# Kernel optimization log

Measured on AMD Instinct MI355X. Metric: run time of the kernel, lower is better.

Reference implementation:

```python
import jax, jax.numpy as jnp
import numpy as np

STEP = 16      # step_size
WIN = 8        # causal window width from attn_mask
NUM_HEADS = 4
LN_EPS = 1e-5


def conv1d(x, w, b, pad, dil):
    # x: [B, Cin, T], w: [Cout, Cin, K] (torch layout)
    y = jax.lax.conv_general_dilated(
        x, w, window_strides=(1,), padding=[(pad, pad)],
        rhs_dilation=(dil,), dimension_numbers=('NCH', 'OIH', 'NCH'))
    return y + b[None, :, None]


def temporal_block(x, w1, b1, w2, b2, wd, bd, dil, pad):
    # Canonical TCN block: conv->chomp->relu (dropout=eval noop) x2 + residual
    T = x.shape[-1]
    out = jax.nn.relu(conv1d(x, w1, b1, pad, dil)[..., :T])
    out = jax.nn.relu(conv1d(out, w2, b2, pad, dil)[..., :T])
    res = x if wd is None else conv1d(x, wd, bd, 0, 1)
    return jax.nn.relu(out + res)


def layer_norm(x, g, b):
    m = x.mean(-1, keepdims=True)
    v = x.var(-1, keepdims=True)
    return (x - m) / jnp.sqrt(v + LN_EPS) * g + b


def setup_inputs() -> dict:
    key = jax.random.key(0)
    NOISE, HID, B, T = 128, 256, 32, 4096
    ks = iter(jax.random.split(key, 48))
    rn = lambda shape, s=0.05: jax.random.normal(next(ks), shape, jnp.float32) * s
    inp = {'z': jax.random.normal(next(ks), (B, NOISE, T), jnp.float32)}
    # TCN block 0: kernel 1, noise_dim -> hidden_dim, with 1x1 downsample
    inp['tb0_w1'] = rn((HID, NOISE, 1)); inp['tb0_b1'] = jnp.zeros(HID)
    inp['tb0_w2'] = rn((HID, HID, 1));   inp['tb0_b2'] = jnp.zeros(HID)
    inp['tb0_wd'] = rn((HID, NOISE, 1)); inp['tb0_bd'] = jnp.zeros(HID)
    # TCN blocks 1..3: kernel 2, dilations 1,2,4, same channels (identity residual)
    for i in (1, 2, 3):
        inp[f'tb{i}_w1'] = rn((HID, HID, 2)); inp[f'tb{i}_b1'] = jnp.zeros(HID)
        inp[f'tb{i}_w2'] = rn((HID, HID, 2)); inp[f'tb{i}_b2'] = jnp.zeros(HID)
    # MultiheadAttention params (torch layout)
    inp['attn_in_w'] = rn((3 * HID, HID)); inp['attn_in_b'] = jnp.zeros(3 * HID)
    inp['attn_out_w'] = rn((HID, HID));    inp['attn_out_b'] = jnp.zeros(HID)
    inp['ln1_g'] = jnp.ones(HID); inp['ln1_b'] = jnp.zeros(HID)
    inp['ln2_g'] = jnp.ones(HID); inp['ln2_b'] = jnp.zeros(HID)
    inp['ffn_w1'] = rn((2 * HID, HID)); inp['ffn_b1'] = jnp.zeros(2 * HID)
    inp['ffn_w2'] = rn((HID, 2 * HID)); inp['ffn_b2'] = jnp.zeros(HID)
    inp['last_w'] = rn((1, HID)); inp['last_b'] = jnp.zeros(1)
    return inp


def reference(z, tb0_w1, tb0_b1, tb0_w2, tb0_b2, tb0_wd, tb0_bd,
              tb1_w1, tb1_b1, tb1_w2, tb1_b2,
              tb2_w1, tb2_b1, tb2_w2, tb2_b2,
              tb3_w1, tb3_b1, tb3_w2, tb3_b2,
              attn_in_w, attn_in_b, attn_out_w, attn_out_b,
              ln1_g, ln1_b, ln2_g, ln2_b,
              ffn_w1, ffn_b1, ffn_w2, ffn_b2,
              last_w, last_b):
    # --- TCN stack ---
    z = temporal_block(z, tb0_w1, tb0_b1, tb0_w2, tb0_b2, tb0_wd, tb0_bd, 1, 0)
    z = temporal_block(z, tb1_w1, tb1_b1, tb1_w2, tb1_b2, None, None, 1, 1)
    z = temporal_block(z, tb2_w1, tb2_b1, tb2_w2, tb2_b2, None, None, 2, 2)
    z = temporal_block(z, tb3_w1, tb3_b1, tb3_w2, tb3_b2, None, None, 4, 4)
    B, C, T = z.shape
    S = T // STEP
    # [B,C,S,STEP] -> [B,STEP,S,C] -> [B*STEP, S, C]
    x = z.reshape(B, C, S, STEP).transpose(0, 3, 2, 1).reshape(B * STEP, S, C)
    # --- causal sliding-window MHA ---
    qkv = x @ attn_in_w.T + attn_in_b
    q, k, v = jnp.split(qkv, 3, axis=-1)
    H, Dh = NUM_HEADS, C // NUM_HEADS
    heads = lambda t: t.reshape(B * STEP, S, H, Dh).transpose(0, 2, 1, 3)
    q, k, v = heads(q), heads(k), heads(v)
    scale = 1.0 / float(np.sqrt(Dh))
    scores = jnp.einsum('bhqd,bhkd->bhqk', q, k) * scale
    i = jnp.arange(S)[:, None]; j = jnp.arange(S)[None, :]
    allowed = (i - j >= 0) & (i - j < WIN)   # masked where i-j<0 or i-j>=8
    scores = jnp.where(allowed, scores, -jnp.inf)
    attn = jax.nn.softmax(scores, axis=-1)
    o = jnp.einsum('bhqk,bhkd->bhqd', attn, v)
    o = o.transpose(0, 2, 1, 3).reshape(B * STEP, S, C)
    o = o @ attn_out_w.T + attn_out_b
    # --- residual + LN + FFN + LN (dropout = eval noop) ---
    x = layer_norm(x + o, ln1_g, ln1_b)
    f = jax.nn.gelu(x @ ffn_w1.T + ffn_b1, approximate=False) @ ffn_w2.T + ffn_b2
    x = layer_norm(x + f, ln2_g, ln2_b)
    # un-fold back to [B, C, T]
    z = x.reshape(B, STEP, S, C).transpose(0, 3, 2, 1).reshape(B, C, T)
    out = z.transpose(0, 2, 1) @ last_w.T + last_b  # [B, T, 1]
    return out.transpose(0, 2, 1)                    # [B, 1, T]
```

## Files before the change

kernel.cpp:

```cpp
#include <hip/hip_runtime.h>
#include <cmath>

#define BB 32
#define TT 4096

typedef unsigned short u16;
typedef __attribute__((ext_vector_type(8))) __bf16 bf16x8;
typedef __attribute__((ext_vector_type(4))) float f32x4;
typedef __attribute__((ext_vector_type(8))) unsigned short u16x8;
typedef __attribute__((ext_vector_type(4))) unsigned short u16x4;
typedef __attribute__((ext_vector_type(2))) unsigned short u16x2;
typedef __attribute__((ext_vector_type(4))) unsigned int u32x4;

typedef __attribute__((address_space(3))) unsigned int lds_uint;
typedef __attribute__((address_space(1))) unsigned int g_uint;

__device__ __forceinline__ void gl_lds16(const void* g, void* l) {
    __builtin_amdgcn_global_load_lds((const g_uint*)g, (lds_uint*)l, 16, 0, 0);
}

__device__ __forceinline__ u16 f2b(float x) {
    unsigned u = __builtin_bit_cast(unsigned, x);
    return (u16)((u + 0x7fffu + ((u >> 16) & 1u)) >> 16);
}
__device__ __forceinline__ float b2f(u16 h) {
    unsigned u = ((unsigned)h) << 16;
    return __builtin_bit_cast(float, u);
}
__device__ __forceinline__ unsigned pkbf(float a, float b) {
    unsigned ua = __builtin_bit_cast(unsigned, a) + 0x8000u;
    unsigned ub = __builtin_bit_cast(unsigned, b) + 0x8000u;
    return __builtin_amdgcn_perm(ub, ua, 0x07060302);
}

enum : int {
  W_TB0_1 = 0,
  W_TB0_2 = 32768,
  W_TB0_D = 98304,
  W_TB1_1_T0 = 131072, W_TB1_1_T1 = 196608,
  W_TB1_2_T0 = 262144, W_TB1_2_T1 = 327680,
  W_TB2_1_T0 = 393216, W_TB2_1_T1 = 458752,
  W_TB2_2_T0 = 524288, W_TB2_2_T1 = 589824,
  W_TB3_1_T0 = 655360, W_TB3_1_T1 = 720896,
  W_TB3_2_T0 = 786432, W_TB3_2_T1 = 851968,
  W_ATTN_IN  = 917504,
  W_ATTN_OUT = 1114112,
  W_FFN1     = 1179648,
  W_FFN2     = 1310720,
};

__global__ __launch_bounds__(256)
void prep_weights(const float* s0, const float* s1, const float* s2,
                  const float* s3, const float* s4, const float* s5,
                  const float* s6, const float* s7, const float* s8,
                  const float* s9, const float* s10, const float* s11,
                  const float* s12, u16* wb)
{
    int seg = blockIdx.y;
    int i = blockIdx.x * 256 + threadIdx.x;
    switch (seg) {
    case 0:  if (i < 32768)  wb[W_TB0_1 + i] = f2b(s0[i]); break;
    case 1:  if (i < 65536)  wb[W_TB0_2 + i] = f2b(s1[i]); break;
    case 2:  if (i < 32768)  wb[W_TB0_D + i] = f2b(s2[i]); break;
    case 3:  if (i < 65536) { wb[W_TB1_1_T0 + i] = f2b(s3[2*i]); wb[W_TB1_1_T1 + i] = f2b(s3[2*i+1]); } break;
    case 4:  if (i < 65536) { wb[W_TB1_2_T0 + i] = f2b(s4[2*i]); wb[W_TB1_2_T1 + i] = f2b(s4[2*i+1]); } break;
    case 5:  if (i < 65536) { wb[W_TB2_1_T0 + i] = f2b(s5[2*i]); wb[W_TB2_1_T1 + i] = f2b(s5[2*i+1]); } break;
    case 6:  if (i < 65536) { wb[W_TB2_2_T0 + i] = f2b(s6[2*i]); wb[W_TB2_2_T1 + i] = f2b(s6[2*i+1]); } break;
    case 7:  if (i < 65536) { wb[W_TB3_1_T0 + i] = f2b(s7[2*i]); wb[W_TB3_1_T1 + i] = f2b(s7[2*i+1]); } break;
    case 8:  if (i < 65536) { wb[W_TB3_2_T0 + i] = f2b(s8[2*i]); wb[W_TB3_2_T1 + i] = f2b(s8[2*i+1]); } break;
    case 9:  if (i < 196608) wb[W_ATTN_IN + i]  = f2b(s9[i]);  break;
    case 10: if (i < 65536)  wb[W_ATTN_OUT + i] = f2b(s10[i]); break;
    case 11: if (i < 131072) wb[W_FFN1 + i]     = f2b(s11[i]); break;
    case 12: if (i < 131072) wb[W_FFN2 + i]     = f2b(s12[i]); break;
    }
}

__global__ __launch_bounds__(256)
void transpose_z(const float* __restrict__ z, u16* __restrict__ Z)
{
    __shared__ u16 tile[64][33];
    const int t0 = blockIdx.x << 6;
    const int c0 = blockIdx.y << 5;
    const int b  = blockIdx.z;
    const int tid = threadIdx.x;
    #pragma unroll
    for (int r = 0; r < 8; r++) {
        int lin = r * 256 + tid;
        int cc = lin >> 6, tt = lin & 63;
        tile[tt][cc] = f2b(z[((size_t)b * 128 + c0 + cc) * TT + t0 + tt]);
    }
    __syncthreads();
    #pragma unroll
    for (int r = 0; r < 8; r++) {
        int lin = r * 256 + tid;
        int tt = lin >> 5, cc = lin & 31;
        Z[((size_t)b * TT + t0 + tt) * 128 + c0 + cc] = tile[tt][cc];
    }
}

__device__ __forceinline__ const bf16x8* lds_frag(const u16* base, int row, int lc) {
    return (const bf16x8*)((const char*)base + row * 128 + (((lc ^ row) & 7) << 4) + ((lc & ~7) << 4));
}

template<int ACT, int RMODE, int EPI>
__global__ __launch_bounds__(256)
void gemm64(const u16* __restrict__ X, const u16* __restrict__ W, int K, int M,
            const float* __restrict__ bias,
            const u16* __restrict__ res, u16* __restrict__ Y,
            const float* __restrict__ g, const float* __restrict__ be,
            const float* __restrict__ lw, const float* __restrict__ lb,
            float* __restrict__ out)
{
    __shared__ __align__(16) char smem[40960];
    u16* Xs = (u16*)smem;
    u16* Ws = (u16*)(smem + 8192);
    float (*CT)[260] = (float(*)[260])smem;

    const int tid = threadIdx.x;
    const int b  = blockIdx.z;
    const int t0 = blockIdx.x << 6;
    const int n0 = blockIdx.y << 8;
    const int lane = tid & 63;
    const int wv = tid >> 6;
    const int wn = wv << 6;
    const int l15 = lane & 15;
    const int quad = lane >> 4;

    const char* xsrc[2]; char* xdst[2];
    #pragma unroll
    for (int u = 0; u < 2; u++) {
        const int c = tid + (u << 8);
        const int r = c >> 3, q = (c & 7) ^ (r & 7);
        xdst[u] = (char*)Xs + c * 16;
        xsrc[u] = (const char*)(X + ((size_t)b * TT + t0 + r) * K + q * 8);
    }
    const char* wsrc[8]; char* wdst[8];
    #pragma unroll
    for (int u = 0; u < 8; u++) {
        const int c = tid + (u << 8);
        const int r = c >> 3, q = (c & 7) ^ (r & 7);
        wdst[u] = (char*)Ws + c * 16;
        wsrc[u] = (const char*)(W + (size_t)(n0 + r) * K + q * 8);
    }

    f32x4 acc[4][4];
    #pragma unroll
    for (int j = 0; j < 4; j++) {
        const f32x4 bj = *(const f32x4*)&bias[n0 + wn + j * 16 + quad * 4];
        #pragma unroll
        for (int i = 0; i < 4; i++) acc[i][j] = bj;
    }

    for (int k0 = 0; k0 < K; k0 += 64) {
        #pragma unroll
        for (int u = 0; u < 2; u++) gl_lds16(xsrc[u] + 2 * k0, xdst[u]);
        #pragma unroll
        for (int u = 0; u < 8; u++) gl_lds16(wsrc[u] + 2 * k0, wdst[u]);
        __syncthreads();
        #pragma unroll
        for (int ks = 0; ks < 2; ks++) {
            const int lc = ks * 4 + quad;
            bf16x8 af[4], bw[4];
            #pragma unroll
            for (int i = 0; i < 4; i++)
                af[i] = *lds_frag(Xs, i * 16 + l15, lc);
            #pragma unroll
            for (int j = 0; j < 4; j++)
                bw[j] = *lds_frag(Ws, wn + j * 16 + l15, lc);
            #pragma unroll
            for (int i = 0; i < 4; i++)
                #pragma unroll
                for (int j = 0; j < 4; j++)
                    acc[i][j] = __builtin_amdgcn_mfma_f32_16x16x32_bf16(bw[j], af[i], acc[i][j], 0, 0, 0);
        }
        __syncthreads();
    }

    #pragma unroll
    for (int h = 0; h < 2; h++) {
        #pragma unroll
        for (int i2 = 0; i2 < 2; i2++) {
            const int tt = i2 * 16 + l15;
            #pragma unroll
            for (int j = 0; j < 4; j++) {
                const int c = wn + j * 16 + quad * 4;
                const int pc = (c + 8 * tt) & 255;
                *(f32x4*)&CT[tt][pc] = acc[h * 2 + i2][j];
            }
        }
        __syncthreads();
        #pragma unroll
        for (int r4 = 0; r4 < 4; r4++) {
            const int lin = (r4 << 8) + tid;
            const int tt = lin >> 5;
            const int ck = lin & 31;
            const int pcc = ((ck + tt) & 31) << 3;
            const int token = t0 + h * 32 + tt;
            const int gc = n0 + ck * 8;
            f32x4 v0 = *(const f32x4*)&CT[tt][pcc];
            f32x4 v1 = *(const f32x4*)&CT[tt][pcc + 4];
            if (RMODE == 1 || EPI >= 1) {
                const u16x8 rv = *(const u16x8*)&res[((size_t)b * TT + token) * 256 + ck * 8];
                #pragma unroll
                for (int e = 0; e < 4; e++) { v0[e] += b2f(rv[e]); v1[e] += b2f(rv[e + 4]); }
            }
            if (EPI == 0) {
                if (ACT == 1) {
                    #pragma unroll
                    for (int e = 0; e < 4; e++) { v0[e] = fmaxf(v0[e], 0.f); v1[e] = fmaxf(v1[e], 0.f); }
                }
                if (ACT == 2) {
                    #pragma unroll
                    for (int e = 0; e < 4; e++) {
                        v0[e] = 0.5f * v0[e] * (1.f + erff(v0[e] * 0.70710678118f));
                        v1[e] = 0.5f * v1[e] * (1.f + erff(v1[e] * 0.70710678118f));
                    }
                }
                u32x4 po;
                po[0] = pkbf(v0[0], v0[1]); po[1] = pkbf(v0[2], v0[3]);
                po[2] = pkbf(v1[0], v1[1]); po[3] = pkbf(v1[2], v1[3]);
                *(u32x4*)&Y[((size_t)b * TT + token) * M + gc] = po;
            } else {
                float s = 0.f, sq = 0.f;
                #pragma unroll
                for (int e = 0; e < 4; e++) {
                    s += v0[e] + v1[e];
                    sq += v0[e] * v0[e] + v1[e] * v1[e];
                }
                #pragma unroll
                for (int off = 16; off >= 1; off >>= 1) {
                    s += __shfl_xor(s, off, 64);
                    sq += __shfl_xor(sq, off, 64);
                }
                const float mean = s * (1.f / 256.f);
                const float var = sq * (1.f / 256.f) - mean * mean;
                const float rstd = rsqrtf(var + 1e-5f);
                const f32x4 g0 = *(const f32x4*)&g[gc];
                const f32x4 g1 = *(const f32x4*)&g[gc + 4];
                const f32x4 be0 = *(const f32x4*)&be[gc];
                const f32x4 be1 = *(const f32x4*)&be[gc + 4];
                f32x4 x0, x1;
                #pragma unroll
                for (int e = 0; e < 4; e++) {
                    x0[e] = (v0[e] - mean) * rstd * g0[e] + be0[e];
                    x1[e] = (v1[e] - mean) * rstd * g1[e] + be1[e];
                }
                if (EPI == 1) {
                    u32x4 po;
                    po[0] = pkbf(x0[0], x0[1]); po[1] = pkbf(x0[2], x0[3]);
                    po[2] = pkbf(x1[0], x1[1]); po[3] = pkbf(x1[2], x1[3]);
                    *(u32x4*)&Y[((size_t)b * TT + token) * 256 + gc] = po;
                } else {
                    const f32x4 w0 = *(const f32x4*)&lw[gc];
                    const f32x4 w1 = *(const f32x4*)&lw[gc + 4];
                    float a = 0.f;
                    #pragma unroll
                    for (int e = 0; e < 4; e++) a += x0[e] * w0[e] + x1[e] * w1[e];
                    #pragma unroll
                    for (int off = 16; off >= 1; off >>= 1) a += __shfl_xor(a, off, 64);
                    if ((lane & 31) == 0) out[(size_t)b * TT + token] = a + lb[0];
                }
            }
        }
        __syncthreads();
    }
}

template<int RMODE>
__global__ __launch_bounds__(256)
void gemm_dual(const u16* __restrict__ X, const u16* __restrict__ W1, int K,
               const u16* __restrict__ W2, int sh,
               const float* __restrict__ bias1,
               const u16* __restrict__ res, u16* __restrict__ Y,
               const u16* __restrict__ zp)
{
    constexpr int XR = 132;
    constexpr int STB = (XR + 256) * 128;
    constexpr int SMB = STB > 33792 ? STB : 33792;
    __shared__ __align__(16) char smem[SMB];
    u16* Xs = (u16*)smem;
    u16* Ws = (u16*)(smem + XR * 128);
    float (*CT)[132] = (float(*)[132])smem;

    const int tid = threadIdx.x;
    const int b  = blockIdx.z;
    const int t0 = blockIdx.x << 7;
    const int n0 = blockIdx.y << 7;
    const int lane = tid & 63;
    const int wv = tid >> 6;
    const int wt = (wv >> 1) << 6;
    const int wn = (wv & 1) << 6;
    const int l15 = lane & 15;
    const int quad = lane >> 4;
    const int shl = sh;

    const char* xsrc[4]; char* xdst[4];
    #pragma unroll
    for (int u = 0; u < 4; u++) {
        const int c = tid + (u << 8);
        const int r = c >> 3, p = c & 7, q = p ^ (r & 7);
        const int st = t0 + r - shl;
        xdst[u] = (char*)Xs + c * 16;
        xsrc[u] = (const char*)((st >= 0 ? (X + ((size_t)b * TT + st) * K) : zp) + q * 8);
    }
    const char* wsrc[8]; char* wdst[8];
    #pragma unroll
    for (int u = 0; u < 8; u++) {
        const int c = tid + (u << 8);
        const int r = c >> 3, p = c & 7, q = p ^ (r & 7);
        wdst[u] = (char*)Ws + c * 16;
        const u16* wb_ = (r >= 128) ? (W2 + (size_t)(n0 + r - 128) * K)
                                    : (W1 + (size_t)(n0 + r) * K);
        wsrc[u] = (const char*)(wb_ + q * 8);
    }
    const u16* hsrc = nullptr; u16* hdst = nullptr;
    if (tid < 8 * shl) {
        const int hr = 128 + (tid >> 3), hp = tid & 7, hq = hp ^ (hr & 7);
        hsrc = X + ((size_t)b * TT + t0 + hr - shl) * K + hq * 8;
        hdst = (u16*)((char*)Xs + (1024 + tid) * 16);
    }

    f32x4 acc[4][4];
    #pragma unroll
    for (int j = 0; j < 4; j++) {
        const f32x4 bj = *(const f32x4*)&bias1[n0 + wn + j * 16 + quad * 4];
        #pragma unroll
        for (int i = 0; i < 4; i++) acc[i][j] = bj;
    }

    for (int k0 = 0; k0 < K; k0 += 64) {
        #pragma unroll
        for (int u = 0; u < 4; u++) gl_lds16(xsrc[u] + 2 * k0, xdst[u]);
        #pragma unroll
        for (int u = 0; u < 8; u++) gl_lds16(wsrc[u] + 2 * k0, wdst[u]);
        if (hdst) *(u16x8*)hdst = *(const u16x8*)(hsrc + k0);
        __syncthreads();
        #pragma unroll
        for (int ks = 0; ks < 2; ks++) {
            bf16x8 af[4], bw[4];
            const int lc = ks * 4 + quad;
            #pragma unroll
            for (int i = 0; i < 4; i++)
                af[i] = *lds_frag(Xs, shl + wt + i * 16 + l15, lc);
            #pragma unroll
            for (int j = 0; j < 4; j++)
                bw[j] = *lds_frag(Ws, wn + j * 16 + l15, lc);
            #pragma unroll
            for (int i = 0; i < 4; i++)
                #pragma unroll
                for (int j = 0; j < 4; j++)
                    acc[i][j] = __builtin_amdgcn_mfma_f32_16x16x32_bf16(bw[j], af[i], acc[i][j], 0, 0, 0);
            #pragma unroll
            for (int i = 0; i < 4; i++)
                af[i] = *lds_frag(Xs, wt + i * 16 + l15, lc);
            #pragma unroll
            for (int j = 0; j < 4; j++)
                bw[j] = *lds_frag(Ws, 128 + wn + j * 16 + l15, lc);
            #pragma unroll
            for (int i = 0; i < 4; i++)
                #pragma unroll
                for (int j = 0; j < 4; j++)
                    acc[i][j] = __builtin_amdgcn_mfma_f32_16x16x32_bf16(bw[j], af[i], acc[i][j], 0, 0, 0);
        }
        __syncthreads();
    }

    #pragma unroll
    for (int h = 0; h < 2; h++) {
        if (wt == h * 64) {
            #pragma unroll
            for (int i = 0; i < 4; i++) {
                const int tt = i * 16 + l15;
                #pragma unroll
                for (int j = 0; j < 4; j++)
                    *(f32x4*)&CT[tt][wn + j * 16 + quad * 4] = acc[i][j];
            }
        }
        __syncthreads();
        #pragma unroll
        for (int r4 = 0; r4 < 4; r4++) {
            const int lin = (r4 << 8) + tid;
            const int tt = lin >> 4;
            const int ck = lin & 15;
            const int gr = t0 + h * 64 + tt;
            const int gc = n0 + ck * 8;
            const size_t oidx = ((size_t)b * TT + gr) * 256 + gc;
            f32x4 v0 = *(const f32x4*)&CT[tt][ck * 8];
            f32x4 v1 = *(const f32x4*)&CT[tt][ck * 8 + 4];
            if (RMODE == 2) {
                const u16x8 rv = *(const u16x8*)&res[oidx];
                #pragma unroll
                for (int e = 0; e < 4; e++) {
                    v0[e] = fmaxf(fmaxf(v0[e], 0.f) + b2f(rv[e]), 0.f);
                    v1[e] = fmaxf(fmaxf(v1[e], 0.f) + b2f(rv[e + 4]), 0.f);
                }
            } else {
                #pragma unroll
                for (int e = 0; e < 4; e++) { v0[e] = fmaxf(v0[e], 0.f); v1[e] = fmaxf(v1[e], 0.f); }
            }
            u32x4 po;
            po[0] = pkbf(v0[0], v0[1]); po[1] = pkbf(v0[2], v0[3]);
            po[2] = pkbf(v1[0], v1[1]); po[3] = pkbf(v1[2], v1[3]);
            *(u32x4*)&Y[oidx] = po;
        }
        if (h == 0) __syncthreads();
    }
}

__global__ __launch_bounds__(256)
void attn_win(const u16* __restrict__ QKV, u16* __restrict__ O)
{
    __shared__ u16 KV[256 * 68];
    const int p = blockIdx.x, h = blockIdx.y, b = blockIdx.z;
    const int tid = threadIdx.x;
    const int s = tid;

    float qv[64];
    {
        size_t qg = ((size_t)b * TT + s * 16 + p) * 768 + h * 64;
        #pragma unroll
        for (int c = 0; c < 8; c++) {
            u16x8 u = *(const u16x8*)&QKV[qg + c * 8];
            #pragma unroll
            for (int j = 0; j < 8; j++) qv[c * 8 + j] = b2f(u[j]);
        }
    }
    for (int u = tid; u < 2048; u += 256) {
        int r = u >> 3, q = u & 7;
        size_t g = ((size_t)b * TT + r * 16 + p) * 768 + 256 + h * 64 + q * 8;
        u16x8 v = *(const u16x8*)&QKV[g];
        u16x4 lo = {v[0], v[1], v[2], v[3]}, hi = {v[4], v[5], v[6], v[7]};
        *(u16x4*)&KV[r * 68 + q * 8] = lo;
        *(u16x4*)&KV[r * 68 + q * 8 + 4] = hi;
    }
    __syncthreads();
    float sc[8];
    float mx = -1e30f;
    #pragma unroll
    for (int kk = 0; kk < 8; kk++) {
        int row = s - 7 + kk;
        float a = -1e30f;
        if (row >= 0) {
            a = 0.f;
            const u16* kr = &KV[row * 68];
            #pragma unroll
            for (int d = 0; d < 32; d++) {
                u16x2 u = *(const u16x2*)&kr[d * 2];
                a += qv[d * 2] * b2f(u[0]) + qv[d * 2 + 1] * b2f(u[1]);
            }
            a *= 0.125f;
        }
        sc[kk] = a;
        mx = fmaxf(mx, a);
    }
    float se = 0.f;
    #pragma unroll
    for (int kk = 0; kk < 8; kk++) {
        float e = (sc[kk] > -1e29f) ? __expf(sc[kk] - mx) : 0.f;
        sc[kk] = e; se += e;
    }
    const float inv = 1.f / se;
    __syncthreads();
    for (int u = tid; u < 2048; u += 256) {
        int r = u >> 3, q = u & 7;
        size_t g = ((size_t)b * TT + r * 16 + p) * 768 + 512 + h * 64 + q * 8;
        u16x8 v = *(const u16x8*)&QKV[g];
        u16x4 lo = {v[0], v[1], v[2], v[3]}, hi = {v[4], v[5], v[6], v[7]};
        *(u16x4*)&KV[r * 68 + q * 8] = lo;
        *(u16x4*)&KV[r * 68 + q * 8 + 4] = hi;
    }
    __syncthreads();
    float ov[64];
    #pragma unroll
    for (int d = 0; d < 64; d++) ov[d] = 0.f;
    #pragma unroll
    for (int kk = 0; kk < 8; kk++) {
        int row = s - 7 + kk;
        if (row >= 0) {
            float w = sc[kk] * inv;
            const u16* vr = &KV[row * 68];
            #pragma unroll
            for (int d = 0; d < 32; d++) {
                u16x2 u = *(const u16x2*)&vr[d * 2];
                ov[d * 2]     += w * b2f(u[0]);
                ov[d * 2 + 1] += w * b2f(u[1]);
            }
        }
    }
    size_t og = ((size_t)b * TT + s * 16 + p) * 256 + h * 64;
    #pragma unroll
    for (int d4 = 0; d4 < 16; d4++) {
        u16x4 o = {f2b(ov[d4 * 4]), f2b(ov[d4 * 4 + 1]), f2b(ov[d4 * 4 + 2]), f2b(ov[d4 * 4 + 3])};
        *(u16x4*)&O[og + d4 * 4] = o;
    }
}

extern "C" void kernel_launch(void* const* d_in, const int* in_sizes, int n_in,
                              void* d_out, int out_size, void* d_ws, size_t ws_size,
                              hipStream_t stream)
{
    const float* z        = (const float*)d_in[0];
    const float* tb0_b1   = (const float*)d_in[2];
    const float* tb0_b2   = (const float*)d_in[4];
    const float* tb0_bd   = (const float*)d_in[6];
    const float* tb1_b1   = (const float*)d_in[8];
    const float* tb1_b2   = (const float*)d_in[10];
    const float* tb2_b1   = (const float*)d_in[12];
    const float* tb2_b2   = (const float*)d_in[14];
    const float* tb3_b1   = (const float*)d_in[16];
    const float* tb3_b2   = (const float*)d_in[18];
    const float* attn_in_b  = (const float*)d_in[20];
    const float* attn_out_b = (const float*)d_in[22];
    const float* ln1_g = (const float*)d_in[23];
    const float* ln1_b = (const float*)d_in[24];
    const float* ln2_g = (const float*)d_in[25];
    const float* ln2_b = (const float*)d_in[26];
    const float* ffn_b1 = (const float*)d_in[28];
    const float* ffn_b2 = (const float*)d_in[30];
    const float* last_w = (const float*)d_in[31];
    const float* last_b = (const float*)d_in[32];
    (void)in_sizes; (void)n_in; (void)out_size;

    const size_t MB = 1ull << 20;
    int Bc = 0;
    for (int c = 32; c >= 1; c >>= 1) {
        if (ws_size >= (4 + 12 * (size_t)c) * MB) { Bc = c; break; }
    }
    if (Bc == 0) return;

    char* ws = (char*)d_ws;
    u16* WBp = (u16*)ws;
    u16* zp  = (u16*)(ws + 3 * MB);
    u16* U1  = (u16*)(ws + 4 * MB);
    u16* U2  = (u16*)(ws + (4 + 2 * (size_t)Bc) * MB);
    u16* U3  = (u16*)(ws + (4 + 4 * (size_t)Bc) * MB);
    u16* Q   = (u16*)(ws + (4 + 6 * (size_t)Bc) * MB);
    u16* Z   = Q;
    u16* F   = Q;
    float* outp = (float*)d_out;

    dim3 b256(256);
    hipMemsetAsync((void*)zp, 0, 4096, stream);
    prep_weights<<<dim3(768, 13), b256, 0, stream>>>(
        (const float*)d_in[1], (const float*)d_in[3], (const float*)d_in[5],
        (const float*)d_in[7], (const float*)d_in[9], (const float*)d_in[11],
        (const float*)d_in[13], (const float*)d_in[15], (const float*)d_in[17],
        (const float*)d_in[19], (const float*)d_in[21],
        (const float*)d_in[27], (const float*)d_in[29], WBp);

    const int nchunk = 32 / Bc;
    for (int c = 0; c < nchunk; c++) {
        const float* zc = z + (size_t)c * Bc * 128 * TT;
        float* oc = outp + (size_t)c * Bc * TT;

        transpose_z<<<dim3(64, 4, Bc), b256, 0, stream>>>(zc, Z);

        gemm64<1, 0, 0><<<dim3(64, 1, Bc), b256, 0, stream>>>(Z, WBp + W_TB0_1, 128, 256,
            tb0_b1, nullptr, U1, nullptr, nullptr, nullptr, nullptr, nullptr);
        gemm64<1, 0, 0><<<dim3(64, 1, Bc), b256, 0, stream>>>(U1, WBp + W_TB0_2, 256, 256,
            tb0_b2, nullptr, U2, nullptr, nullptr, nullptr, nullptr, nullptr);
        gemm64<1, 1, 0><<<dim3(64, 1, Bc), b256, 0, stream>>>(Z, WBp + W_TB0_D, 128, 256,
            tb0_bd, U2, U3, nullptr, nullptr, nullptr, nullptr, nullptr);
        gemm_dual<0><<<dim3(32, 2, Bc), b256, 0, stream>>>(U3, WBp + W_TB1_1_T1, 256,
            WBp + W_TB1_1_T0, 1, tb1_b1, nullptr, U1, zp);
        gemm_dual<2><<<dim3(32, 2, Bc), b256, 0, stream>>>(U1, WBp + W_TB1_2_T1, 256,
            WBp + W_TB1_2_T0, 1, tb1_b2, U3, U2, zp);
        gemm_dual<0><<<dim3(32, 2, Bc), b256, 0, stream>>>(U2, WBp + W_TB2_1_T1, 256,
            WBp + W_TB2_1_T0, 2, tb2_b1, nullptr, U1, zp);
        gemm_dual<2><<<dim3(32, 2, Bc), b256, 0, stream>>>(U1, WBp + W_TB2_2_T1, 256,
            WBp + W_TB2_2_T0, 2, tb2_b2, U2, U3, zp);
        gemm_dual<0><<<dim3(32, 2, Bc), b256, 0, stream>>>(U3, WBp + W_TB3_1_T1, 256,
            WBp + W_TB3_1_T0, 4, tb3_b1, nullptr, U1, zp);
        gemm_dual<2><<<dim3(32, 2, Bc), b256, 0, stream>>>(U1, WBp + W_TB3_2_T1, 256,
            WBp + W_TB3_2_T0, 4, tb3_b2, U3, U2, zp);
        gemm64<0, 0, 0><<<dim3(64, 3, Bc), b256, 0, stream>>>(U2, WBp + W_ATTN_IN, 256, 768,
            attn_in_b, nullptr, Q, nullptr, nullptr, nullptr, nullptr, nullptr);
        attn_win<<<dim3(16, 4, Bc), b256, 0, stream>>>(Q, U3);
        gemm64<0, 0, 1><<<dim3(64, 1, Bc), b256, 0, stream>>>(U3, WBp + W_ATTN_OUT, 256, 256,
            attn_out_b, U2, U1, ln1_g, ln1_b, nullptr, nullptr, nullptr);
        gemm64<2, 0, 0><<<dim3(64, 2, Bc), b256, 0, stream>>>(U1, WBp + W_FFN1, 256, 512,
            ffn_b1, nullptr, F, nullptr, nullptr, nullptr, nullptr, nullptr);
        gemm64<0, 0, 2><<<dim3(64, 1, Bc), b256, 0, stream>>>(F, WBp + W_FFN2, 512, 256,
            ffn_b2, U1, nullptr, ln2_g, ln2_b, last_w, last_b, oc);
    }
}
```

Before: 912.0 us.

## Load GEMM fragments directly from global memory and merge dual-tap conv kernel

Replaces the LDS-staged async global-to-LDS tiling with direct per-lane global loads of MFMA fragments, fully unrolled over a compile-time K. It also folds the two-tap dilated conv kernel into the same templated GEMM, which now uses 64-token tiles and reads a shifted X row for the second tap. The aim is to drop LDS staging and barriers from the main loop. In exchange, global loads are uncoalesced across lanes and weights are re-read per wave with no shared reuse, so it leans heavily on cache.

```diff
diff --git a/kernel.cpp b/kernel.cpp
--- a/kernel.cpp
+++ b/kernel.cpp
@@ -11,13 +11,6 @@
 typedef __attribute__((ext_vector_type(4))) unsigned short u16x4;
 typedef __attribute__((ext_vector_type(2))) unsigned short u16x2;
 typedef __attribute__((ext_vector_type(4))) unsigned int u32x4;
-
-typedef __attribute__((address_space(3))) unsigned int lds_uint;
-typedef __attribute__((address_space(1))) unsigned int g_uint;
-
-__device__ __forceinline__ void gl_lds16(const void* g, void* l) {
-    __builtin_amdgcn_global_load_lds((const g_uint*)g, (lds_uint*)l, 16, 0, 0);
-}
 
 __device__ __forceinline__ u16 f2b(float x) {
     unsigned u = __builtin_bit_cast(unsigned, x);
@@ -98,23 +91,17 @@
     }
 }
 
-__device__ __forceinline__ const bf16x8* lds_frag(const u16* base, int row, int lc) {
-    return (const bf16x8*)((const char*)base + row * 128 + (((lc ^ row) & 7) << 4) + ((lc & ~7) << 4));
-}
-
-template<int ACT, int RMODE, int EPI>
+template<int ACT, int RMODE, int EPI, bool DUAL, int KT>
 __global__ __launch_bounds__(256)
-void gemm64(const u16* __restrict__ X, const u16* __restrict__ W, int K, int M,
-            const float* __restrict__ bias,
-            const u16* __restrict__ res, u16* __restrict__ Y,
-            const float* __restrict__ g, const float* __restrict__ be,
-            const float* __restrict__ lw, const float* __restrict__ lb,
-            float* __restrict__ out)
+void gemmd(const u16* __restrict__ X, const u16* __restrict__ W1, int M,
+           const u16* __restrict__ W2, int sh,
+           const float* __restrict__ bias,
+           const u16* __restrict__ res, u16* __restrict__ Y,
+           const float* __restrict__ g, const float* __restrict__ be,
+           const float* __restrict__ lw, const float* __restrict__ lb,
+           float* __restrict__ out, const u16* __restrict__ zp)
 {
-    __shared__ __align__(16) char smem[40960];
-    u16* Xs = (u16*)smem;
-    u16* Ws = (u16*)(smem + 8192);
-    float (*CT)[260] = (float(*)[260])smem;
+    __shared__ float CT[32][260];
 
     const int tid = threadIdx.x;
     const int b  = blockIdx.z;
@@ -126,21 +113,24 @@
     const int l15 = lane & 15;
     const int quad = lane >> 4;
 
-    const char* xsrc[2]; char* xdst[2];
-    #pragma unroll
-    for (int u = 0; u < 2; u++) {
-        const int c = tid + (u << 8);
-        const int r = c >> 3, q = (c & 7) ^ (r & 7);
-        xdst[u] = (char*)Xs + c * 16;
-        xsrc[u] = (const char*)(X + ((size_t)b * TT + t0 + r) * K + q * 8);
-    }
-    const char* wsrc[8]; char* wdst[8];
-    #pragma unroll
-    for (int u = 0; u < 8; u++) {
-        const int c = tid + (u << 8);
-        const int r = c >> 3, q = (c & 7) ^ (r & 7);
-        wdst[u] = (char*)Ws + c * 16;
-        wsrc[u] = (const char*)(W + (size_t)(n0 + r) * K + q * 8);
+    const u16* xrow[4];
+    const u16* xrow2[4];
+    const u16* wrow[4];
+    const u16* wrow2[4];
+    #pragma unroll
+    for (int i = 0; i < 4; i++) {
+        const int t = t0 + i * 16 + l15;
+        xrow[i] = X + ((size_t)b * TT + t) * KT + quad * 8;
+        if (DUAL) {
+            const int ts = t - sh;
+            xrow2[i] = (ts >= 0) ? (X + ((size_t)b * TT + ts) * KT + quad * 8) : zp;
+        }
+    }
+    #pragma unroll
+    for (int j = 0; j < 4; j++) {
+        const int m = n0 + wn + j * 16 + l15;
+        wrow[j] = W1 + (size_t)m * KT + quad * 8;
+        if (DUAL) wrow2[j] = W2 + (size_t)m * KT + quad * 8;
     }
 
     f32x4 acc[4][4];
@@ -151,33 +141,36 @@
         for (int i = 0; i < 4; i++) acc[i][j] = bj;
     }
 
-    for (int k0 = 0; k0 < K; k0 += 64) {
-        #pragma unroll
-        for (int u = 0; u < 2; u++) gl_lds16(xsrc[u] + 2 * k0, xdst[u]);
-        #pragma unroll
-        for (int u = 0; u < 8; u++) gl_lds16(wsrc[u] + 2 * k0, wdst[u]);
-        __syncthreads();
-        #pragma unroll
-        for (int ks = 0; ks < 2; ks++) {
-            const int lc = ks * 4 + quad;
-            bf16x8 af[4], bw[4];
+    #pragma unroll
+    for (int ks = 0; ks < KT / 32; ks++) {
+        const int ko = ks * 32;
+        bf16x8 af[4], bw[4];
+        #pragma unroll
+        for (int i = 0; i < 4; i++) af[i] = *(const bf16x8*)(xrow[i] + ko);
+        #pragma unroll
+        for (int j = 0; j < 4; j++) bw[j] = *(const bf16x8*)(wrow[j] + ko);
+        #pragma unroll
+        for (int i = 0; i < 4; i++)
+            #pragma unroll
+            for (int j = 0; j < 4; j++)
+                acc[i][j] = __builtin_amdgcn_mfma_f32_16x16x32_bf16(bw[j], af[i], acc[i][j], 0, 0, 0);
+        if (DUAL) {
+            bf16x8 af2[4], bw2[4];
+            #pragma unroll
+            for (int i = 0; i < 4; i++) af2[i] = *(const bf16x8*)(xrow2[i] + ko);
+            #pragma unroll
+            for (int j = 0; j < 4; j++) bw2[j] = *(const bf16x8*)(wrow2[j] + ko);
             #pragma unroll
             for (int i = 0; i < 4; i++)
-                af[i] = *lds_frag(Xs, i * 16 + l15, lc);
-            #pragma unroll
-            for (int j = 0; j < 4; j++)
-                bw[j] = *lds_frag(Ws, wn + j * 16 + l15, lc);
-            #pragma unroll
-            for (int i = 0; i < 4; i++)
                 #pragma unroll
                 for (int j = 0; j < 4; j++)
-                    acc[i][j] = __builtin_amdgcn_mfma_f32_16x16x32_bf16(bw[j], af[i], acc[i][j], 0, 0, 0);
-        }
-        __syncthreads();
+                    acc[i][j] = __builtin_amdgcn_mfma_f32_16x16x32_bf16(bw2[j], af2[i], acc[i][j], 0, 0, 0);
+        }
     }
 
     #pragma unroll
     for (int h = 0; h < 2; h++) {
+        if (h) __syncthreads();
         #pragma unroll
         for (int i2 = 0; i2 < 2; i2++) {
             const int tt = i2 * 16 + l15;
@@ -204,16 +197,26 @@
                 #pragma unroll
                 for (int e = 0; e < 4; e++) { v0[e] += b2f(rv[e]); v1[e] += b2f(rv[e + 4]); }
             }
+            if (RMODE == 2) {
+                const u16x8 rv = *(const u16x8*)&res[((size_t)b * TT + token) * 256 + ck * 8];
+                #pragma unroll
+                for (int e = 0; e < 4; e++) {
+                    v0[e] = fmaxf(fmaxf(v0[e], 0.f) + b2f(rv[e]), 0.f);
+                    v1[e] = fmaxf(fmaxf(v1[e], 0.f) + b2f(rv[e + 4]), 0.f);
+                }
+            }
             if (EPI == 0) {
-                if (ACT == 1) {
-                    #pragma unroll
-                    for (int e = 0; e < 4; e++) { v0[e] = fmaxf(v0[e], 0.f); v1[e] = fmaxf(v1[e], 0.f); }
-                }
-                if (ACT == 2) {
-                    #pragma unroll
-                    for (int e = 0; e < 4; e++) {
-                        v0[e] = 0.5f * v0[e] * (1.f + erff(v0[e] * 0.70710678118f));
-                        v1[e] = 0.5f * v1[e] * (1.f + erff(v1[e] * 0.70710678118f));
+                if (RMODE != 2) {
+                    if (ACT == 1) {
+                        #pragma unroll
+                        for (int e = 0; e < 4; e++) { v0[e] = fmaxf(v0[e], 0.f); v1[e] = fmaxf(v1[e], 0.f); }
+                    }
+                    if (ACT == 2) {
+                        #pragma unroll
+                        for (int e = 0; e < 4; e++) {
+                            v0[e] = 0.5f * v0[e] * (1.f + erff(v0[e] * 0.70710678118f));
+                            v1[e] = 0.5f * v1[e] * (1.f + erff(v1[e] * 0.70710678118f));
+                        }
                     }
                 }
                 u32x4 po;
@@ -262,148 +265,6 @@
                 }
             }
         }
-        __syncthreads();
-    }
-}
-
-template<int RMODE>
-__global__ __launch_bounds__(256)
-void gemm_dual(const u16* __restrict__ X, const u16* __restrict__ W1, int K,
-               const u16* __restrict__ W2, int sh,
-               const float* __restrict__ bias1,
-               const u16* __restrict__ res, u16* __restrict__ Y,
-               const u16* __restrict__ zp)
-{
-    constexpr int XR = 132;
-    constexpr int STB = (XR + 256) * 128;
-    constexpr int SMB = STB > 33792 ? STB : 33792;
-    __shared__ __align__(16) char smem[SMB];
-    u16* Xs = (u16*)smem;
-    u16* Ws = (u16*)(smem + XR * 128);
-    float (*CT)[132] = (float(*)[132])smem;
-
-    const int tid = threadIdx.x;
-    const int b  = blockIdx.z;
-    const int t0 = blockIdx.x << 7;
-    const int n0 = blockIdx.y << 7;
-    const int lane = tid & 63;
-    const int wv = tid >> 6;
-    const int wt = (wv >> 1) << 6;
-    const int wn = (wv & 1) << 6;
-    const int l15 = lane & 15;
-    const int quad = lane >> 4;
-    const int shl = sh;
-
-    const char* xsrc[4]; char* xdst[4];
-    #pragma unroll
-    for (int u = 0; u < 4; u++) {
-        const int c = tid + (u << 8);
-        const int r = c >> 3, p = c & 7, q = p ^ (r & 7);
-        const int st = t0 + r - shl;
-        xdst[u] = (char*)Xs + c * 16;
-        xsrc[u] = (const char*)((st >= 0 ? (X + ((size_t)b * TT + st) * K) : zp) + q * 8);
-    }
-    const char* wsrc[8]; char* wdst[8];
-    #pragma unroll
-    for (int u = 0; u < 8; u++) {
-        const int c = tid + (u << 8);
-        const int r = c >> 3, p = c & 7, q = p ^ (r & 7);
-        wdst[u] = (char*)Ws + c * 16;
-        const u16* wb_ = (r >= 128) ? (W2 + (size_t)(n0 + r - 128) * K)
-                                    : (W1 + (size_t)(n0 + r) * K);
-        wsrc[u] = (const char*)(wb_ + q * 8);
-    }
-    const u16* hsrc = nullptr; u16* hdst = nullptr;
-    if (tid < 8 * shl) {
-        const int hr = 128 + (tid >> 3), hp = tid & 7, hq = hp ^ (hr & 7);
-        hsrc = X + ((size_t)b * TT + t0 + hr - shl) * K + hq * 8;
-        hdst = (u16*)((char*)Xs + (1024 + tid) * 16);
-    }
-
-    f32x4 acc[4][4];
-    #pragma unroll
-    for (int j = 0; j < 4; j++) {
-        const f32x4 bj = *(const f32x4*)&bias1[n0 + wn + j * 16 + quad * 4];
-        #pragma unroll
-        for (int i = 0; i < 4; i++) acc[i][j] = bj;
-    }
-
-    for (int k0 = 0; k0 < K; k0 += 64) {
-        #pragma unroll
-        for (int u = 0; u < 4; u++) gl_lds16(xsrc[u] + 2 * k0, xdst[u]);
-        #pragma unroll
-        for (int u = 0; u < 8; u++) gl_lds16(wsrc[u] + 2 * k0, wdst[u]);
-        if (hdst) *(u16x8*)hdst = *(const u16x8*)(hsrc + k0);
-        __syncthreads();
-        #pragma unroll
-        for (int ks = 0; ks < 2; ks++) {
-            bf16x8 af[4], bw[4];
-            const int lc = ks * 4 + quad;
-            #pragma unroll
-            for (int i = 0; i < 4; i++)
-                af[i] = *lds_frag(Xs, shl + wt + i * 16 + l15, lc);
-            #pragma unroll
-            for (int j = 0; j < 4; j++)
-                bw[j] = *lds_frag(Ws, wn + j * 16 + l15, lc);
-            #pragma unroll
-            for (int i = 0; i < 4; i++)
-                #pragma unroll
-                for (int j = 0; j < 4; j++)
-                    acc[i][j] = __builtin_amdgcn_mfma_f32_16x16x32_bf16(bw[j], af[i], acc[i][j], 0, 0, 0);
-            #pragma unroll
-            for (int i = 0; i < 4; i++)
-                af[i] = *lds_frag(Xs, wt + i * 16 + l15, lc);
-            #pragma unroll
-            for (int j = 0; j < 4; j++)
-                bw[j] = *lds_frag(Ws, 128 + wn + j * 16 + l15, lc);
-            #pragma unroll
-            for (int i = 0; i < 4; i++)
-                #pragma unroll
-                for (int j = 0; j < 4; j++)
-                    acc[i][j] = __builtin_amdgcn_mfma_f32_16x16x32_bf16(bw[j], af[i], acc[i][j], 0, 0, 0);
-        }
-        __syncthreads();
-    }
-
-    #pragma unroll
-    for (int h = 0; h < 2; h++) {
-        if (wt == h * 64) {
-            #pragma unroll
-            for (int i = 0; i < 4; i++) {
-                const int tt = i * 16 + l15;
-                #pragma unroll
-                for (int j = 0; j < 4; j++)
-                    *(f32x4*)&CT[tt][wn + j * 16 + quad * 4] = acc[i][j];
-            }
-        }
-        __syncthreads();
-        #pragma unroll
-        for (int r4 = 0; r4 < 4; r4++) {
-            const int lin = (r4 << 8) + tid;
-            const int tt = lin >> 4;
-            const int ck = lin & 15;
-            const int gr = t0 + h * 64 + tt;
-            const int gc = n0 + ck * 8;
-            const size_t oidx = ((size_t)b * TT + gr) * 256 + gc;
-            f32x4 v0 = *(const f32x4*)&CT[tt][ck * 8];
-            f32x4 v1 = *(const f32x4*)&CT[tt][ck * 8 + 4];
-            if (RMODE == 2) {
-                const u16x8 rv = *(const u16x8*)&res[oidx];
-                #pragma unroll
-                for (int e = 0; e < 4; e++) {
-                    v0[e] = fmaxf(fmaxf(v0[e], 0.f) + b2f(rv[e]), 0.f);
-                    v1[e] = fmaxf(fmaxf(v1[e], 0.f) + b2f(rv[e + 4]), 0.f);
-                }
-            } else {
-                #pragma unroll
-                for (int e = 0; e < 4; e++) { v0[e] = fmaxf(v0[e], 0.f); v1[e] = fmaxf(v1[e], 0.f); }
-            }
-            u32x4 po;
-            po[0] = pkbf(v0[0], v0[1]); po[1] = pkbf(v0[2], v0[3]);
-            po[2] = pkbf(v1[0], v1[1]); po[3] = pkbf(v1[2], v1[3]);
-            *(u32x4*)&Y[oidx] = po;
-        }
-        if (h == 0) __syncthreads();
     }
 }
 
@@ -555,32 +416,32 @@
 
         transpose_z<<<dim3(64, 4, Bc), b256, 0, stream>>>(zc, Z);
 
-        gemm64<1, 0, 0><<<dim3(64, 1, Bc), b256, 0, stream>>>(Z, WBp + W_TB0_1, 128, 256,
-            tb0_b1, nullptr, U1, nullptr, nullptr, nullptr, nullptr, nullptr);
-        gemm64<1, 0, 0><<<dim3(64, 1, Bc), b256, 0, stream>>>(U1, WBp + W_TB0_2, 256, 256,
-            tb0_b2, nullptr, U2, nullptr, nullptr, nullptr, nullptr, nullptr);
-        gemm64<1, 1, 0><<<dim3(64, 1, Bc), b256, 0, stream>>>(Z, WBp + W_TB0_D, 128, 256,
-            tb0_bd, U2, U3, nullptr, nullptr, nullptr, nullptr, nullptr);
-        gemm_dual<0><<<dim3(32, 2, Bc), b256, 0, stream>>>(U3, WBp + W_TB1_1_T1, 256,
-            WBp + W_TB1_1_T0, 1, tb1_b1, nullptr, U1, zp);
-        gemm_dual<2><<<dim3(32, 2, Bc), b256, 0, stream>>>(U1, WBp + W_TB1_2_T1, 256,
-            WBp + W_TB1_2_T0, 1, tb1_b2, U3, U2, zp);
-        gemm_dual<0><<<dim3(32, 2, Bc), b256, 0, stream>>>(U2, WBp + W_TB2_1_T1, 256,
-            WBp + W_TB2_1_T0, 2, tb2_b1, nullptr, U1, zp);
-        gemm_dual<2><<<dim3(32, 2, Bc), b256, 0, stream>>>(U1, WBp + W_TB2_2_T1, 256,
-            WBp + W_TB2_2_T0, 2, tb2_b2, U2, U3, zp);
-        gemm_dual<0><<<dim3(32, 2, Bc), b256, 0, stream>>>(U3, WBp + W_TB3_1_T1, 256,
-            WBp + W_TB3_1_T0, 4, tb3_b1, nullptr, U1, zp);
-        gemm_dual<2><<<dim3(32, 2, Bc), b256, 0, stream>>>(U1, WBp + W_TB3_2_T1, 256,
-            WBp + W_TB3_2_T0, 4, tb3_b2, U3, U2, zp);
-        gemm64<0, 0, 0><<<dim3(64, 3, Bc), b256, 0, stream>>>(U2, WBp + W_ATTN_IN, 256, 768,
-            attn_in_b, nullptr, Q, nullptr, nullptr, nullptr, nullptr, nullptr);
+        gemmd<1, 0, 0, false, 128><<<dim3(64, 1, Bc), b256, 0, stream>>>(Z, WBp + W_TB0_1, 256,
+            nullptr, 0, tb0_b1, nullptr, U1, nullptr, nullptr, nullptr, nullptr, nullptr, zp);
+        gemmd<1, 0, 0, false, 256><<<dim3(64, 1, Bc), b256, 0, stream>>>(U1, WBp + W_TB0_2, 256,
+            nullptr, 0, tb0_b2, nullptr, U2, nullptr, nullptr, nullptr, nullptr, nullptr, zp);
+        gemmd<1, 1, 0, false, 128><<<dim3(64, 1, Bc), b256, 0, stream>>>(Z, WBp + W_TB0_D, 256,
+            nullptr, 0, tb0_bd, U2, U3, nullptr, nullptr, nullptr, nullptr, nullptr, zp);
+        gemmd<1, 0, 0, true, 256><<<dim3(64, 1, Bc), b256, 0, stream>>>(U3, WBp + W_TB1_1_T1, 256,
+            WBp + W_TB1_1_T0, 1, tb1_b1, nullptr, U1, nullptr, nullptr, nullptr, nullptr, nullptr, zp);
+        gemmd<1, 2, 0, true, 256><<<dim3(64, 1, Bc), b256, 0, stream>>>(U1, WBp + W_TB1_2_T1, 256,
+            WBp + W_TB1_2_T0, 1, tb1_b2, U3, U2, nullptr, nullptr, nullptr, nullptr, nullptr, zp);
+        gemmd<1, 0, 0, true, 256><<<dim3(64, 1, Bc), b256, 0, stream>>>(U2, WBp + W_TB2_1_T1, 256,
+            WBp + W_TB2_1_T0, 2, tb2_b1, nullptr, U1, nullptr, nullptr, nullptr, nullptr, nullptr, zp);
+        gemmd<1, 2, 0, true, 256><<<dim3(64, 1, Bc), b256, 0, stream>>>(U1, WBp + W_TB2_2_T1, 256,
+            WBp + W_TB2_2_T0, 2, tb2_b2, U2, U3, nullptr, nullptr, nullptr, nullptr, nullptr, zp);
+        gemmd<1, 0, 0, true, 256><<<dim3(64, 1, Bc), b256, 0, stream>>>(U3, WBp + W_TB3_1_T1, 256,
+            WBp + W_TB3_1_T0, 4, tb3_b1, nullptr, U1, nullptr, nullptr, nullptr, nullptr, nullptr, zp);
+        gemmd<1, 2, 0, true, 256><<<dim3(64, 1, Bc), b256, 0, stream>>>(U1, WBp + W_TB3_2_T1, 256,
+            WBp + W_TB3_2_T0, 4, tb3_b2, U3, U2, nullptr, nullptr, nullptr, nullptr, nullptr, zp);
+        gemmd<0, 0, 0, false, 256><<<dim3(64, 3, Bc), b256, 0, stream>>>(U2, WBp + W_ATTN_IN, 768,
+            nullptr, 0, attn_in_b, nullptr, Q, nullptr, nullptr, nullptr, nullptr, nullptr, zp);
         attn_win<<<dim3(16, 4, Bc), b256, 0, stream>>>(Q, U3);
-        gemm64<0, 0, 1><<<dim3(64, 1, Bc), b256, 0, stream>>>(U3, WBp + W_ATTN_OUT, 256, 256,
-            attn_out_b, U2, U1, ln1_g, ln1_b, nullptr, nullptr, nullptr);
-        gemm64<2, 0, 0><<<dim3(64, 2, Bc), b256, 0, stream>>>(U1, WBp + W_FFN1, 256, 512,
-            ffn_b1, nullptr, F, nullptr, nullptr, nullptr, nullptr, nullptr);
-        gemm64<0, 0, 2><<<dim3(64, 1, Bc), b256, 0, stream>>>(F, WBp + W_FFN2, 512, 256,
-            ffn_b2, U1, nullptr, ln2_g, ln2_b, last_w, last_b, oc);
-    }
-}
+        gemmd<0, 0, 1, false, 256><<<dim3(64, 1, Bc), b256, 0, stream>>>(U3, WBp + W_ATTN_OUT, 256,
+            attn_out_b ? nullptr : nullptr, 0, attn_out_b, U2, U1, ln1_g, ln1_b, nullptr, nullptr, nullptr, zp);
+        gemmd<2, 0, 0, false, 256><<<dim3(64, 2, Bc), b256, 0, stream>>>(U1, WBp + W_FFN1, 512,
+            nullptr, 0, ffn_b1, nullptr, F, nullptr, nullptr, nullptr, nullptr, nullptr, zp);
+        gemmd<0, 0, 2, false, 512><<<dim3(64, 1, Bc), b256, 0, stream>>>(F, WBp + W_FFN2, 256,
+            nullptr, 0, ffn_b2, U1, nullptr, ln2_g, ln2_b, last_w, last_b, oc, zp);
+    }
+}
```

Measured after the change: 1.718 ms. 1.88x slower.
